# Kernel tuning notes

Hardware: AMD Instinct MI355X
Metric: run time of the kernel (lower is better)

## Reference

```python
import jax, jax.numpy as jnp
import numpy as np

DIM = 2048; H = 16; QLR = 512; KVLR = 512
NOPE = 128; ROPE = 64; VHD = 128
QKHD = NOPE + ROPE
SCALE = QKHD ** -0.5
EPS = 1.1920929e-07  # torch RMSNorm default eps = finfo(float32).eps
B = 1; S = 2048

def _rmsnorm(x, w):
    return x * jax.lax.rsqrt(jnp.mean(x * x, axis=-1, keepdims=True) + EPS) * w

def _rope(x, cos, sin):
    # x: [b, s, h, d]; cos/sin: [s, d//2] (consecutive-pair complex rotation)
    b, s, h, d = x.shape
    x2 = x.reshape(b, s, h, d // 2, 2)
    x0, x1 = x2[..., 0], x2[..., 1]
    c = cos[None, :, None, :]; sn = sin[None, :, None, :]
    y = jnp.stack([x0 * c - x1 * sn, x0 * sn + x1 * c], axis=-1)
    return y.reshape(b, s, h, d)

def setup_inputs() -> dict:
    key = jax.random.key(0)
    ks = jax.random.split(key, 12)
    def lin(k, fan_in, fan_out):
        bound = 1.0 / np.sqrt(fan_in)
        kw, kb = jax.random.split(k)
        w = jax.random.uniform(kw, (fan_out, fan_in), jnp.float32, -bound, bound)
        b = jax.random.uniform(kb, (fan_out,), jnp.float32, -bound, bound)
        return w, b
    x = jax.random.normal(ks[0], (B, S, DIM), jnp.float32)
    theta = jax.random.uniform(ks[1], (S, ROPE // 2), jnp.float32, 0.0, 2 * np.pi)
    freqs_cos = jnp.cos(theta); freqs_sin = jnp.sin(theta)
    mask = jnp.where(jnp.triu(jnp.ones((S, S), bool), k=1), jnp.float32(-1e9), jnp.float32(0.0))
    wq_a_w, wq_a_b = lin(ks[2], DIM, QLR)
    q_norm_w = jnp.ones((QLR,), jnp.float32)
    wq_b_w, wq_b_b = lin(ks[3], QLR, H * QKHD)
    wkv_a_w, wkv_a_b = lin(ks[4], DIM, KVLR + ROPE)
    kv_norm_w = jnp.ones((KVLR,), jnp.float32)
    wkv_b_w, wkv_b_b = lin(ks[5], KVLR, H * (NOPE + VHD))
    wo_w, wo_b = lin(ks[6], H * VHD, DIM)
    return {"x": x, "start_pos": 0, "freqs_cos": freqs_cos, "freqs_sin": freqs_sin,
            "mask": mask, "wq_a_w": wq_a_w, "wq_a_b": wq_a_b, "q_norm_w": q_norm_w,
            "wq_b_w": wq_b_w, "wq_b_b": wq_b_b, "wkv_a_w": wkv_a_w, "wkv_a_b": wkv_a_b,
            "kv_norm_w": kv_norm_w, "wkv_b_w": wkv_b_w, "wkv_b_b": wkv_b_b,
            "wo_w": wo_w, "wo_b": wo_b}

def reference(x, start_pos, freqs_cos, freqs_sin, mask,
              wq_a_w, wq_a_b, q_norm_w, wq_b_w, wq_b_b,
              wkv_a_w, wkv_a_b, kv_norm_w, wkv_b_w, wkv_b_b, wo_w, wo_b):
    bsz, seqlen, _ = x.shape
    # low-rank query: wq_b(q_norm(wq_a(x)))
    q = _rmsnorm(x @ wq_a_w.T + wq_a_b, q_norm_w) @ wq_b_w.T + wq_b_b
    q = q.reshape(bsz, seqlen, H, QKHD)
    q_nope, q_pe = q[..., :NOPE], q[..., NOPE:]
    q_pe = _rope(q_pe, freqs_cos, freqs_sin)
    kv = x @ wkv_a_w.T + wkv_a_b
    kv_lat, k_pe = kv[..., :KVLR], kv[..., KVLR:]
    k_pe = _rope(k_pe[:, :, None, :], freqs_cos, freqs_sin)  # [b,s,1,ROPE]
    q = jnp.concatenate([q_nope, q_pe], axis=-1)
    kvb = (_rmsnorm(kv_lat, kv_norm_w) @ wkv_b_w.T + wkv_b_b).reshape(bsz, seqlen, H, NOPE + VHD)
    k_nope, v = kvb[..., :NOPE], kvb[..., NOPE:]
    k = jnp.concatenate([k_nope, jnp.broadcast_to(k_pe, (bsz, seqlen, H, ROPE))], axis=-1)
    # prefill (start_pos=0): cache[:end_pos] == freshly written k/v
    scores = jnp.einsum('bshd,bthd->bsht', q, k) * SCALE
    scores = scores + mask[None, :, None, :]
    probs = jax.nn.softmax(scores.astype(jnp.float32), axis=-1).astype(x.dtype)
    out = jnp.einsum('bsht,bthd->bshd', probs, v).reshape(bsz, seqlen, H * VHD)
    return out @ wo_w.T + wo_b
```

## Files before the change

### kernel.cpp

```cpp
#include <hip/hip_runtime.h>
#include <hip/hip_bf16.h>

typedef __attribute__((ext_vector_type(8))) short short8x;
typedef __attribute__((ext_vector_type(4))) short short4x;
typedef __attribute__((ext_vector_type(4))) float float4x;
typedef __hip_bfloat16 bf16;

#define EPS_F 1.1920929e-07f
#define SCALE_F 0.07216878364870323f

__device__ inline float rdv(const void* p, size_t i, int f32) {
  return f32 ? ((const float*)p)[i] : __bfloat162float(((const bf16*)p)[i]);
}

__device__ inline int4 pack8(const float* s) {
  unsigned short h[8];
#pragma unroll
  for (int t = 0; t < 8; t++) {
    bf16 b = __float2bfloat16(s[t]);
    __builtin_memcpy(&h[t], &b, 2);
  }
  int4 r;
  r.x = (int)((unsigned)h[0] | ((unsigned)h[1] << 16));
  r.y = (int)((unsigned)h[2] | ((unsigned)h[3] << 16));
  r.z = (int)((unsigned)h[4] | ((unsigned)h[5] << 16));
  r.w = (int)((unsigned)h[6] | ((unsigned)h[7] << 16));
  return r;
}

typedef __attribute__((address_space(1))) const unsigned int gu32;
typedef __attribute__((address_space(3))) unsigned int lu32;
__device__ __forceinline__ void gload16(const void* g, void* l) {
  __builtin_amdgcn_global_load_lds((gu32*)g, (lu32*)l, 16, 0, 0);
}

__global__ __launch_bounds__(256) void detect_dtype(const unsigned short* __restrict__ x,
                                                    int* __restrict__ flag) {
  int tid = threadIdx.x;
  int cnt = 0;
#pragma unroll
  for (int i = 0; i < 4; i++) {
    unsigned short u = x[tid * 4 + i];
    int e = (u >> 7) & 0xFF;
    cnt += (e >= 118 && e <= 130) ? 1 : 0;
  }
#pragma unroll
  for (int off = 1; off < 64; off <<= 1) cnt += __shfl_xor(cnt, off);
  __shared__ int red[4];
  if ((tid & 63) == 0) red[tid >> 6] = cnt;
  __syncthreads();
  if (tid == 0) flag[0] = ((red[0] + red[1] + red[2] + red[3]) > 768) ? 0 : 1;
}

__global__ __launch_bounds__(256) void sentinel_kernel(bf16* out, int n) {
  int i = blockIdx.x * 256 + threadIdx.x;
  if (i < n) out[i] = __float2bfloat16(1000.0f);
}

template<int OMODE, bool A_DYN>
__device__ __forceinline__ void gemm128_body(
    const void* __restrict__ A, const void* __restrict__ W,
    const void* __restrict__ bias, void* __restrict__ Cout,
    int M, int N, int K, int f32in, int bx, int by)
{
  __shared__ int4 As4[128 * 4];
  __shared__ int4 Bs4[128 * 4];
  const int tid = threadIdx.x, lane = tid & 63, wave = tid >> 6;
  const int grp = lane >> 4, l16 = lane & 15;
  const int m0 = bx * 128, n0 = by * 128;
  const int wm = (wave & 1) * 64, wn = (wave >> 1) * 64;
  float4x acc[4][4] = {};
  for (int k0 = 0; k0 < K; k0 += 32) {
    if (!f32in) {
#pragma unroll
      for (int j = 0; j < 2; j++) {
        int row = wave * 32 + j * 16 + (lane >> 2);
        int cs = (lane & 3) ^ ((row >> 1) & 3);
        gload16((const bf16*)A + (size_t)(m0 + row) * K + k0 + cs * 8,
                &As4[(wave * 32 + j * 16) * 4]);
        gload16((const bf16*)W + (size_t)(n0 + row) * K + k0 + cs * 8,
                &Bs4[(wave * 32 + j * 16) * 4]);
      }
    } else {
#pragma unroll
      for (int i = 0; i < 2; i++) {
        int ch = tid + i * 256;
        int row = ch >> 2, c = ch & 3;
        int cs = c ^ ((row >> 1) & 3);
        size_t aoff = (size_t)(m0 + row) * K + k0 + cs * 8;
        size_t boff = (size_t)(n0 + row) * K + k0 + cs * 8;
        As4[row * 4 + c] = A_DYN ? pack8((const float*)A + aoff)
                                 : *(const int4*)((const bf16*)A + aoff);
        Bs4[row * 4 + c] = pack8((const float*)W + boff);
      }
    }
    __syncthreads();
    short8x af[4], bfr[4];
#pragma unroll
    for (int i = 0; i < 4; i++) {
      int ra = wm + i * 16 + l16;
      int rb = wn + i * 16 + l16;
      af[i]  = *(const short8x*)&As4[ra * 4 + (grp ^ ((ra >> 1) & 3))];
      bfr[i] = *(const short8x*)&Bs4[rb * 4 + (grp ^ ((rb >> 1) & 3))];
    }
#pragma unroll
    for (int i = 0; i < 4; i++)
#pragma unroll
      for (int j = 0; j < 4; j++)
        acc[i][j] = __builtin_amdgcn_mfma_f32_16x16x32_bf16(af[i], bfr[j], acc[i][j], 0, 0, 0);
    __syncthreads();
  }
#pragma unroll
  for (int j = 0; j < 4; j++) {
    int gn = n0 + wn + j * 16 + l16;
    float bv = rdv(bias, gn, f32in);
#pragma unroll
    for (int i = 0; i < 4; i++) {
      int gm0 = m0 + wm + i * 16 + grp * 4;
#pragma unroll
      for (int r = 0; r < 4; r++) {
        float v = acc[i][j][r] + bv;
        size_t idx = (size_t)(gm0 + r) * N + gn;
        if (OMODE == 0)      ((float*)Cout)[idx] = v;
        else if (OMODE == 1) ((bf16*)Cout)[idx] = __float2bfloat16(v);
        else {
          if (f32in) ((float*)Cout)[idx] = v;
          else       ((bf16*)Cout)[idx] = __float2bfloat16(v);
        }
      }
    }
  }
}

template<int OMODE, bool A_DYN>
__global__ __launch_bounds__(256) void gemm128(
    const void* __restrict__ A, const void* __restrict__ W,
    const void* __restrict__ bias, void* __restrict__ Cout,
    int M, int N, int K, const int* __restrict__ flagp)
{
  gemm128_body<OMODE, A_DYN>(A, W, bias, Cout, M, N, K, flagp[0],
                             blockIdx.x, blockIdx.y);
}

__global__ __launch_bounds__(256) void gemmB_dual(
    const void* __restrict__ A0, const void* __restrict__ A1,
    const void* __restrict__ W0, const void* __restrict__ W1,
    const void* __restrict__ b0, const void* __restrict__ b1,
    void* __restrict__ C0, void* __restrict__ C1,
    const int* __restrict__ flagp)
{
  const int z = blockIdx.z;
  if (z == 0 && blockIdx.y >= 24) return;
  const void* A = z ? A1 : A0;
  const void* W = z ? W1 : W0;
  const void* bias = z ? b1 : b0;
  void* C = z ? C1 : C0;
  const int N = z ? 4096 : 3072;
  gemm128_body<1, false>(A, W, bias, C, 2048, N, 512, flagp[0],
                         blockIdx.x, blockIdx.y);
}

template<int OMODE, bool A_DYN>
__device__ __forceinline__ void gemm64_body(
    const void* __restrict__ A, const void* __restrict__ W,
    const void* __restrict__ bias, void* __restrict__ Cout,
    int M, int N, int K, int f32in, int bx, int by)
{
  __shared__ int4 As4[64 * 4];
  __shared__ int4 Bs4[64 * 4];
  const int tid = threadIdx.x, lane = tid & 63, wave = tid >> 6;
  const int grp = lane >> 4, l16 = lane & 15;
  const int m0 = bx * 64, n0 = by * 64;
  const int wm = (wave & 1) * 32, wn = (wave >> 1) * 32;
  float4x acc[2][2] = {};
  for (int k0 = 0; k0 < K; k0 += 32) {
    if (!f32in) {
      int row = wave * 16 + (lane >> 2);
      int cs = (lane & 3) ^ ((row >> 1) & 3);
      gload16((const bf16*)A + (size_t)(m0 + row) * K + k0 + cs * 8,
              &As4[wave * 16 * 4]);
      gload16((const bf16*)W + (size_t)(n0 + row) * K + k0 + cs * 8,
              &Bs4[wave * 16 * 4]);
    } else {
      int row = tid >> 2, c = tid & 3;
      int cs = c ^ ((row >> 1) & 3);
      size_t aoff = (size_t)(m0 + row) * K + k0 + cs * 8;
      size_t boff = (size_t)(n0 + row) * K + k0 + cs * 8;
      As4[row * 4 + c] = A_DYN ? pack8((const float*)A + aoff)
                               : *(const int4*)((const bf16*)A + aoff);
      Bs4[row * 4 + c] = pack8((const float*)W + boff);
    }
    __syncthreads();
    short8x af[2], bfr[2];
#pragma unroll
    for (int i = 0; i < 2; i++) {
      int ra = wm + i * 16 + l16;
      int rb = wn + i * 16 + l16;
      af[i]  = *(const short8x*)&As4[ra * 4 + (grp ^ ((ra >> 1) & 3))];
      bfr[i] = *(const short8x*)&Bs4[rb * 4 + (grp ^ ((rb >> 1) & 3))];
    }
#pragma unroll
    for (int i = 0; i < 2; i++)
#pragma unroll
      for (int j = 0; j < 2; j++)
        acc[i][j] = __builtin_amdgcn_mfma_f32_16x16x32_bf16(af[i], bfr[j], acc[i][j], 0, 0, 0);
    __syncthreads();
  }
#pragma unroll
  for (int j = 0; j < 2; j++) {
    int gn = n0 + wn + j * 16 + l16;
    float bv = rdv(bias, gn, f32in);
#pragma unroll
    for (int i = 0; i < 2; i++) {
      int gm0 = m0 + wm + i * 16 + grp * 4;
#pragma unroll
      for (int r = 0; r < 4; r++) {
        float v = acc[i][j][r] + bv;
        size_t idx = (size_t)(gm0 + r) * N + gn;
        if (OMODE == 0)      ((float*)Cout)[idx] = v;
        else if (OMODE == 1) ((bf16*)Cout)[idx] = __float2bfloat16(v);
        else {
          if (f32in) ((float*)Cout)[idx] = v;
          else       ((bf16*)Cout)[idx] = __float2bfloat16(v);
        }
      }
    }
  }
}

__global__ __launch_bounds__(256) void gemmA_dual(
    const void* __restrict__ A,
    const void* __restrict__ W0, const void* __restrict__ W1,
    const void* __restrict__ b0, const void* __restrict__ b1,
    float* __restrict__ C0, float* __restrict__ C1,
    const int* __restrict__ flagp)
{
  const int z = blockIdx.z;
  const int N = z ? 576 : 512;
  if (blockIdx.y * 64 >= N) return;
  const void* W = z ? W1 : W0;
  const void* bias = z ? b1 : b0;
  float* C = z ? C1 : C0;
  gemm64_body<0, true>(A, W, bias, C, 2048, N, 2048, flagp[0],
                       blockIdx.x, blockIdx.y);
}

__global__ __launch_bounds__(256) void norms_merged(
    const float* __restrict__ q_a, const float* __restrict__ kv_a,
    const void* __restrict__ qw, const void* __restrict__ kvw,
    const void* __restrict__ cosb, const void* __restrict__ sinb,
    bf16* __restrict__ qn, bf16* __restrict__ kvn, bf16* __restrict__ kpe,
    const int* __restrict__ flagp)
{
  const int f32in = flagp[0];
  const int b = blockIdx.x, tid = threadIdx.x;
  __shared__ float red[4];
  if (b < 2048) {
    const int s = b;
    const float* row = q_a + (size_t)s * 512;
    float v0 = row[tid], v1 = row[tid + 256];
    float ss = v0 * v0 + v1 * v1;
#pragma unroll
    for (int off = 1; off < 64; off <<= 1) ss += __shfl_xor(ss, off);
    if ((tid & 63) == 0) red[tid >> 6] = ss;
    __syncthreads();
    float tot = red[0] + red[1] + red[2] + red[3];
    float scale = rsqrtf(tot * (1.0f / 512.0f) + EPS_F);
    qn[(size_t)s * 512 + tid]       = __float2bfloat16(v0 * scale * rdv(qw, tid, f32in));
    qn[(size_t)s * 512 + tid + 256] = __float2bfloat16(v1 * scale * rdv(qw, tid + 256, f32in));
  } else {
    const int s = b - 2048;
    const float* row = kv_a + (size_t)s * 576;
    float v0 = row[tid], v1 = row[tid + 256];
    float ss = v0 * v0 + v1 * v1;
#pragma unroll
    for (int off = 1; off < 64; off <<= 1) ss += __shfl_xor(ss, off);
    if ((tid & 63) == 0) red[tid >> 6] = ss;
    __syncthreads();
    float tot = red[0] + red[1] + red[2] + red[3];
    float scale = rsqrtf(tot * (1.0f / 512.0f) + EPS_F);
    kvn[(size_t)s * 512 + tid]       = __float2bfloat16(v0 * scale * rdv(kvw, tid, f32in));
    kvn[(size_t)s * 512 + tid + 256] = __float2bfloat16(v1 * scale * rdv(kvw, tid + 256, f32in));
    if (tid < 32) {
      float x0 = row[512 + 2 * tid], x1 = row[512 + 2 * tid + 1];
      float c  = rdv(cosb, (size_t)s * 32 + tid, f32in);
      float sn = rdv(sinb, (size_t)s * 32 + tid, f32in);
      kpe[s * 64 + 2 * tid]     = __float2bfloat16(x0 * c - x1 * sn);
      kpe[s * 64 + 2 * tid + 1] = __float2bfloat16(x0 * sn + x1 * c);
    }
  }
}

__global__ __launch_bounds__(256) void rope_vt_merged(
    bf16* __restrict__ q, const void* __restrict__ cosb,
    const void* __restrict__ sinb, const bf16* __restrict__ kvb,
    bf16* __restrict__ Vt, const int* __restrict__ flagp)
{
  const int b = blockIdx.x, tid = threadIdx.x;
  __shared__ __align__(16) bf16 tile[64][136];
  if (b < 2048) {
    const int f32in = flagp[0];
    const int s = b;
#pragma unroll
    for (int it = 0; it < 2; it++) {
      int p = tid + it * 256;
      int hh = p >> 5, jj = p & 31;
      bf16* src = q + (size_t)s * 3072 + hh * 192 + 128 + 2 * jj;
      float x0 = __bfloat162float(src[0]);
      float x1 = __bfloat162float(src[1]);
      float c  = rdv(cosb, (size_t)s * 32 + jj, f32in);
      float sn = rdv(sinb, (size_t)s * 32 + jj, f32in);
      src[0] = __float2bfloat16(x0 * c - x1 * sn);
      src[1] = __float2bfloat16(x0 * sn + x1 * c);
    }
  } else {
    const int hb = b - 2048;
    const int h = hb & 15;
    const int t0 = (hb >> 4) * 64;
#pragma unroll
    for (int i = 0; i < 4; i++) {
      int chunk = tid + i * 256;
      int row = chunk >> 4;
      int c8 = (chunk & 15) * 8;
      *(int4*)&tile[row][c8] =
          *(const int4*)(kvb + (size_t)(t0 + row) * 4096 + h * 256 + 128 + c8);
    }
    __syncthreads();
#pragma unroll
    for (int i = 0; i < 32; i++) {
      int idx = tid + i * 256;
      int d = idx >> 6;
      int t = idx & 63;
      Vt[((size_t)h * 128 + d) * 2048 + t0 + t] = tile[t][d];
    }
  }
}

__global__ __launch_bounds__(256) void attn_kernel(
    const bf16* __restrict__ Q, const bf16* __restrict__ kvb,
    const bf16* __restrict__ kpe, const bf16* __restrict__ Vt,
    bf16* __restrict__ Out)
{
  __shared__ __align__(16) bf16 Ks[64 * 200];
  __shared__ __align__(16) bf16 Vs[128 * 72];
  __shared__ __align__(16) bf16 plds[4][16 * 68];
  const int b = blockIdx.x;
  const int h = b & 15;
  const int tt = (b >> 4) & 15;
  const int q0 = ((b >> 8) ? (31 - tt) : tt) * 64;
  const int tid = threadIdx.x;
  const int wave = tid >> 6;
  const int lane = tid & 63;
  const int grp = lane >> 4, l16 = lane & 15;
  const int qrt = q0 + wave * 16;
  const bf16* Qbase = Q + (size_t)(qrt + l16) * 3072 + h * 192;
  short8x qf[6];
#pragma unroll
  for (int c = 0; c < 6; c++)
    qf[c] = *(const short8x*)(Qbase + c * 32 + grp * 8);
  float m_run[4], l_run[4];
  float4x o_acc[8] = {};
#pragma unroll
  for (int r = 0; r < 4; r++) { m_run[r] = -__builtin_inff(); l_run[r] = 0.f; }
  bf16* pl = &plds[wave][0];
  for (int t0 = 0; t0 <= q0; t0 += 64) {
#pragma unroll
    for (int i = 0; i < 4; i++) {
      int ch = tid + i * 256;
      int row = ch >> 4, c = ch & 15;
      *(int4*)&Ks[row * 200 + c * 8] =
          *(const int4*)(kvb + (size_t)(t0 + row) * 4096 + h * 256 + c * 8);
    }
#pragma unroll
    for (int i = 0; i < 2; i++) {
      int ch = tid + i * 256;
      int row = ch >> 3, c = ch & 7;
      *(int4*)&Ks[row * 200 + 128 + c * 8] =
          *(const int4*)(kpe + (size_t)(t0 + row) * 64 + c * 8);
    }
#pragma unroll
    for (int i = 0; i < 4; i++) {
      int ch = tid + i * 256;
      int row = ch >> 3, c = ch & 7;
      *(int4*)&Vs[row * 72 + c * 8] =
          *(const int4*)(Vt + ((size_t)h * 128 + row) * 2048 + t0 + c * 8);
    }
    __syncthreads();
    float4x sacc[4] = {};
#pragma unroll
    for (int n = 0; n < 4; n++) {
      const bf16* Kb = &Ks[(n * 16 + l16) * 200 + grp * 8];
#pragma unroll
      for (int c = 0; c < 6; c++) {
        short8x kf = *(const short8x*)(Kb + c * 32);
        sacc[n] = __builtin_amdgcn_mfma_f32_16x16x32_bf16(qf[c], kf, sacc[n], 0, 0, 0);
      }
    }
    float pv[4][4], alpha[4];
#pragma unroll
    for (int r = 0; r < 4; r++) {
      const int s_row = qrt + grp * 4 + r;
      float p0[4];
      float mx = -__builtin_inff();
#pragma unroll
      for (int n = 0; n < 4; n++) {
        int t = t0 + n * 16 + l16;
        float v = sacc[n][r] * SCALE_F;
        v = (t > s_row) ? -1.0e9f : v;
        p0[n] = v;
        mx = fmaxf(mx, v);
      }
      mx = fmaxf(mx, __shfl_xor(mx, 1));
      mx = fmaxf(mx, __shfl_xor(mx, 2));
      mx = fmaxf(mx, __shfl_xor(mx, 4));
      mx = fmaxf(mx, __shfl_xor(mx, 8));
      float m_new = fmaxf(m_run[r], mx);
      float a = __expf(m_run[r] - m_new);
      m_run[r] = m_new;
      float sum = 0.f;
#pragma unroll
      for (int n = 0; n < 4; n++) {
        float e = __expf(p0[n] - m_new);
        pv[n][r] = e;
        sum += e;
      }
      sum += __shfl_xor(sum, 1);
      sum += __shfl_xor(sum, 2);
      sum += __shfl_xor(sum, 4);
      sum += __shfl_xor(sum, 8);
      l_run[r] = l_run[r] * a + sum;
      alpha[r] = a;
    }
#pragma unroll
    for (int n = 0; n < 8; n++)
#pragma unroll
      for (int r = 0; r < 4; r++)
        o_acc[n][r] *= alpha[r];
#pragma unroll
    for (int n = 0; n < 4; n++)
#pragma unroll
      for (int r = 0; r < 4; r++)
        pl[(grp * 4 + r) * 68 + n * 16 + l16] = __float2bfloat16(pv[n][r]);
#pragma unroll
    for (int c = 0; c < 2; c++) {
      union { short4x h4[2]; short8x v8; } pk;
      const bf16* pp = pl + l16 * 68 + c * 32 + grp * 8;
      pk.h4[0] = *(const short4x*)(pp);
      pk.h4[1] = *(const short4x*)(pp + 4);
#pragma unroll
      for (int n = 0; n < 8; n++) {
        short8x vf = *(const short8x*)&Vs[(size_t)(n * 16 + l16) * 72 + c * 32 + grp * 8];
        o_acc[n] = __builtin_amdgcn_mfma_f32_16x16x32_bf16(pk.v8, vf, o_acc[n], 0, 0, 0);
      }
    }
    __syncthreads();
  }
  float inv[4];
#pragma unroll
  for (int r = 0; r < 4; r++) inv[r] = 1.0f / l_run[r];
#pragma unroll
  for (int n = 0; n < 8; n++)
#pragma unroll
    for (int r = 0; r < 4; r++) {
      int s_row = qrt + grp * 4 + r;
      Out[(size_t)s_row * 2048 + h * 128 + n * 16 + l16] =
          __float2bfloat16(o_acc[n][r] * inv[r]);
    }
}

extern "C" void kernel_launch(void* const* d_in, const int* in_sizes, int n_in,
                              void* d_out, int out_size, void* d_ws, size_t ws_size,
                              hipStream_t stream) {
  const void* x        = d_in[0];
  const void* fcos     = d_in[2];
  const void* fsin     = d_in[3];
  const void* wq_a_w   = d_in[5];
  const void* wq_a_b   = d_in[6];
  const void* q_norm_w = d_in[7];
  const void* wq_b_w   = d_in[8];
  const void* wq_b_b   = d_in[9];
  const void* wkv_a_w  = d_in[10];
  const void* wkv_a_b  = d_in[11];
  const void* kv_norm_w= d_in[12];
  const void* wkv_b_w  = d_in[13];
  const void* wkv_b_b  = d_in[14];
  const void* wo_w     = d_in[15];
  const void* wo_b     = d_in[16];

  const size_t KB = 1024, MB = 1024 * 1024;
  if (ws_size < 46 * MB) {
    sentinel_kernel<<<(out_size + 255) / 256, 256, 0, stream>>>((bf16*)d_out, out_size);
    return;
  }
  char* ws = (char*)d_ws;
  bf16*  kpe    = (bf16*)(ws);
  int*   flag   = (int*)(ws + 256 * KB);
  bf16*  qbuf   = (bf16*)(ws + 512 * KB);
  bf16*  kvb    = (bf16*)(ws + 12 * MB + 512 * KB);
  bf16*  Vt     = (bf16*)(ws + 28 * MB + 512 * KB);
  bf16*  attnout= (bf16*)(ws + 36 * MB + 512 * KB);
  float* q_a    = (float*)(ws + 28 * MB + 512 * KB);
  float* kv_a   = (float*)(ws + 32 * MB + 512 * KB);
  bf16*  qn     = (bf16*)(ws + 37 * MB);
  bf16*  kvn    = (bf16*)(ws + 39 * MB);

  dim3 blk(256);
  detect_dtype<<<1, blk, 0, stream>>>((const unsigned short*)x, flag);
  gemmA_dual<<<dim3(32, 9, 2), blk, 0, stream>>>(
      x, wq_a_w, wkv_a_w, wq_a_b, wkv_a_b, q_a, kv_a, flag);
  norms_merged<<<4096, blk, 0, stream>>>(
      q_a, kv_a, q_norm_w, kv_norm_w, fcos, fsin, qn, kvn, kpe, flag);
  gemmB_dual<<<dim3(16, 32, 2), blk, 0, stream>>>(
      qn, kvn, wq_b_w, wkv_b_w, wq_b_b, wkv_b_b, qbuf, kvb, flag);
  rope_vt_merged<<<2560, blk, 0, stream>>>(qbuf, fcos, fsin, kvb, Vt, flag);
  attn_kernel<<<dim3(512), blk, 0, stream>>>(qbuf, kvb, kpe, Vt, attnout);
  gemm128<2, false><<<dim3(16, 16), blk, 0, stream>>>(
      attnout, wo_w, wo_b, d_out, 2048, 2048, 2048, flag);
}
```

Measured before the change: 384.3 us.

## Split-K the Wo projection and first-stage projections to raise parallelism

Adds k-range and bias-enable parameters to the shared 128- and 64-tile GEMM bodies so one launch can compute two K halves into separate fp32 partial buffers. The output projection now launches twice as many blocks and uses a new reduce kernel that sums the partials, converts the dtype and writes the output. The first x-projection GEMM is split the same way, and the norm kernel sums the two partials as it reads them. The aim is to fill more compute units on the 2048-deep reductions. The cost is extra fp32 partial traffic, one more kernel launch, and a rearranged workspace layout that reuses buffers once they are dead.

```diff
diff --git a/kernel.cpp b/kernel.cpp
--- a/kernel.cpp
+++ b/kernel.cpp
@@ -61,7 +61,8 @@
 __device__ __forceinline__ void gemm128_body(
     const void* __restrict__ A, const void* __restrict__ W,
     const void* __restrict__ bias, void* __restrict__ Cout,
-    int M, int N, int K, int f32in, int bx, int by)
+    int M, int N, int K, int f32in, int bx, int by,
+    int kbeg, int kend, int addbias)
 {
   __shared__ int4 As4[128 * 4];
   __shared__ int4 Bs4[128 * 4];
@@ -70,7 +71,7 @@
   const int m0 = bx * 128, n0 = by * 128;
   const int wm = (wave & 1) * 64, wn = (wave >> 1) * 64;
   float4x acc[4][4] = {};
-  for (int k0 = 0; k0 < K; k0 += 32) {
+  for (int k0 = kbeg; k0 < kend; k0 += 32) {
     if (!f32in) {
 #pragma unroll
       for (int j = 0; j < 2; j++) {
@@ -113,7 +114,7 @@
 #pragma unroll
   for (int j = 0; j < 4; j++) {
     int gn = n0 + wn + j * 16 + l16;
-    float bv = rdv(bias, gn, f32in);
+    float bv = addbias ? rdv(bias, gn, f32in) : 0.0f;
 #pragma unroll
     for (int i = 0; i < 4; i++) {
       int gm0 = m0 + wm + i * 16 + grp * 4;
@@ -132,16 +133,6 @@
   }
 }
 
-template<int OMODE, bool A_DYN>
-__global__ __launch_bounds__(256) void gemm128(
-    const void* __restrict__ A, const void* __restrict__ W,
-    const void* __restrict__ bias, void* __restrict__ Cout,
-    int M, int N, int K, const int* __restrict__ flagp)
-{
-  gemm128_body<OMODE, A_DYN>(A, W, bias, Cout, M, N, K, flagp[0],
-                             blockIdx.x, blockIdx.y);
-}
-
 __global__ __launch_bounds__(256) void gemmB_dual(
     const void* __restrict__ A0, const void* __restrict__ A1,
     const void* __restrict__ W0, const void* __restrict__ W1,
@@ -157,14 +148,50 @@
   void* C = z ? C1 : C0;
   const int N = z ? 4096 : 3072;
   gemm128_body<1, false>(A, W, bias, C, 2048, N, 512, flagp[0],
-                         blockIdx.x, blockIdx.y);
+                         blockIdx.x, blockIdx.y, 0, 512, 1);
+}
+
+__global__ __launch_bounds__(256) void gemmWo_sk(
+    const void* __restrict__ A, const void* __restrict__ W,
+    const void* __restrict__ bias, float* __restrict__ part,
+    const int* __restrict__ flagp)
+{
+  const int z = blockIdx.z;
+  gemm128_body<0, false>(A, W, bias, part + (size_t)z * 2048 * 2048,
+                         2048, 2048, 2048, flagp[0],
+                         blockIdx.x, blockIdx.y, z * 1024, z * 1024 + 1024, z == 0);
+}
+
+__global__ __launch_bounds__(256) void reduce_out(
+    const float* __restrict__ p0, const float* __restrict__ p1,
+    void* __restrict__ out, const int* __restrict__ flagp)
+{
+  const int f32in = flagp[0];
+  size_t i = ((size_t)blockIdx.x * 256 + threadIdx.x) * 4;
+  float4 a = *(const float4*)(p0 + i);
+  float4 b = *(const float4*)(p1 + i);
+  a.x += b.x; a.y += b.y; a.z += b.z; a.w += b.w;
+  if (f32in) {
+    *(float4*)((float*)out + i) = a;
+  } else {
+    unsigned short h[4];
+    bf16 t0 = __float2bfloat16(a.x); __builtin_memcpy(&h[0], &t0, 2);
+    bf16 t1 = __float2bfloat16(a.y); __builtin_memcpy(&h[1], &t1, 2);
+    bf16 t2 = __float2bfloat16(a.z); __builtin_memcpy(&h[2], &t2, 2);
+    bf16 t3 = __float2bfloat16(a.w); __builtin_memcpy(&h[3], &t3, 2);
+    int2 v;
+    v.x = (int)((unsigned)h[0] | ((unsigned)h[1] << 16));
+    v.y = (int)((unsigned)h[2] | ((unsigned)h[3] << 16));
+    *(int2*)((bf16*)out + i) = v;
+  }
 }
 
 template<int OMODE, bool A_DYN>
 __device__ __forceinline__ void gemm64_body(
     const void* __restrict__ A, const void* __restrict__ W,
     const void* __restrict__ bias, void* __restrict__ Cout,
-    int M, int N, int K, int f32in, int bx, int by)
+    int M, int N, int K, int f32in, int bx, int by,
+    int kbeg, int kend, int addbias)
 {
   __shared__ int4 As4[64 * 4];
   __shared__ int4 Bs4[64 * 4];
@@ -173,7 +200,7 @@
   const int m0 = bx * 64, n0 = by * 64;
   const int wm = (wave & 1) * 32, wn = (wave >> 1) * 32;
   float4x acc[2][2] = {};
-  for (int k0 = 0; k0 < K; k0 += 32) {
+  for (int k0 = kbeg; k0 < kend; k0 += 32) {
     if (!f32in) {
       int row = wave * 16 + (lane >> 2);
       int cs = (lane & 3) ^ ((row >> 1) & 3);
@@ -209,7 +236,7 @@
 #pragma unroll
   for (int j = 0; j < 2; j++) {
     int gn = n0 + wn + j * 16 + l16;
-    float bv = rdv(bias, gn, f32in);
+    float bv = addbias ? rdv(bias, gn, f32in) : 0.0f;
 #pragma unroll
     for (int i = 0; i < 2; i++) {
       int gm0 = m0 + wm + i * 16 + grp * 4;
@@ -228,7 +255,7 @@
   }
 }
 
-__global__ __launch_bounds__(256) void gemmA_dual(
+__global__ __launch_bounds__(256) void gemmA_sk(
     const void* __restrict__ A,
     const void* __restrict__ W0, const void* __restrict__ W1,
     const void* __restrict__ b0, const void* __restrict__ b1,
@@ -236,17 +263,20 @@
     const int* __restrict__ flagp)
 {
   const int z = blockIdx.z;
-  const int N = z ? 576 : 512;
+  const int mat = z >> 1, kh = z & 1;
+  const int N = mat ? 576 : 512;
   if (blockIdx.y * 64 >= N) return;
-  const void* W = z ? W1 : W0;
-  const void* bias = z ? b1 : b0;
-  float* C = z ? C1 : C0;
+  const void* W = mat ? W1 : W0;
+  const void* bias = mat ? b1 : b0;
+  float* C = (mat ? C1 : C0) + (size_t)kh * 2048 * N;
   gemm64_body<0, true>(A, W, bias, C, 2048, N, 2048, flagp[0],
-                       blockIdx.x, blockIdx.y);
+                       blockIdx.x, blockIdx.y,
+                       kh * 1024, kh * 1024 + 1024, kh == 0);
 }
 
 __global__ __launch_bounds__(256) void norms_merged(
-    const float* __restrict__ q_a, const float* __restrict__ kv_a,
+    const float* __restrict__ q_a0, const float* __restrict__ q_a1,
+    const float* __restrict__ kv_a0, const float* __restrict__ kv_a1,
     const void* __restrict__ qw, const void* __restrict__ kvw,
     const void* __restrict__ cosb, const void* __restrict__ sinb,
     bf16* __restrict__ qn, bf16* __restrict__ kvn, bf16* __restrict__ kpe,
@@ -257,8 +287,9 @@
   __shared__ float red[4];
   if (b < 2048) {
     const int s = b;
-    const float* row = q_a + (size_t)s * 512;
-    float v0 = row[tid], v1 = row[tid + 256];
+    size_t base = (size_t)s * 512;
+    float v0 = q_a0[base + tid] + q_a1[base + tid];
+    float v1 = q_a0[base + tid + 256] + q_a1[base + tid + 256];
     float ss = v0 * v0 + v1 * v1;
 #pragma unroll
     for (int off = 1; off < 64; off <<= 1) ss += __shfl_xor(ss, off);
@@ -266,12 +297,13 @@
     __syncthreads();
     float tot = red[0] + red[1] + red[2] + red[3];
     float scale = rsqrtf(tot * (1.0f / 512.0f) + EPS_F);
-    qn[(size_t)s * 512 + tid]       = __float2bfloat16(v0 * scale * rdv(qw, tid, f32in));
-    qn[(size_t)s * 512 + tid + 256] = __float2bfloat16(v1 * scale * rdv(qw, tid + 256, f32in));
+    qn[base + tid]       = __float2bfloat16(v0 * scale * rdv(qw, tid, f32in));
+    qn[base + tid + 256] = __float2bfloat16(v1 * scale * rdv(qw, tid + 256, f32in));
   } else {
     const int s = b - 2048;
-    const float* row = kv_a + (size_t)s * 576;
-    float v0 = row[tid], v1 = row[tid + 256];
+    size_t base = (size_t)s * 576;
+    float v0 = kv_a0[base + tid] + kv_a1[base + tid];
+    float v1 = kv_a0[base + tid + 256] + kv_a1[base + tid + 256];
     float ss = v0 * v0 + v1 * v1;
 #pragma unroll
     for (int off = 1; off < 64; off <<= 1) ss += __shfl_xor(ss, off);
@@ -282,7 +314,8 @@
     kvn[(size_t)s * 512 + tid]       = __float2bfloat16(v0 * scale * rdv(kvw, tid, f32in));
     kvn[(size_t)s * 512 + tid + 256] = __float2bfloat16(v1 * scale * rdv(kvw, tid + 256, f32in));
     if (tid < 32) {
-      float x0 = row[512 + 2 * tid], x1 = row[512 + 2 * tid + 1];
+      float x0 = kv_a0[base + 512 + 2 * tid] + kv_a1[base + 512 + 2 * tid];
+      float x1 = kv_a0[base + 512 + 2 * tid + 1] + kv_a1[base + 512 + 2 * tid + 1];
       float c  = rdv(cosb, (size_t)s * 32 + tid, f32in);
       float sn = rdv(sinb, (size_t)s * 32 + tid, f32in);
       kpe[s * 64 + 2 * tid]     = __float2bfloat16(x0 * c - x1 * sn);
@@ -499,21 +532,25 @@
   bf16*  kvb    = (bf16*)(ws + 12 * MB + 512 * KB);
   bf16*  Vt     = (bf16*)(ws + 28 * MB + 512 * KB);
   bf16*  attnout= (bf16*)(ws + 36 * MB + 512 * KB);
-  float* q_a    = (float*)(ws + 28 * MB + 512 * KB);
-  float* kv_a   = (float*)(ws + 32 * MB + 512 * KB);
-  bf16*  qn     = (bf16*)(ws + 37 * MB);
-  bf16*  kvn    = (bf16*)(ws + 39 * MB);
+  float* kv_a0  = (float*)(ws + 512 * KB);
+  float* kv_a1  = (float*)(ws + 5 * MB);
+  float* q_a0   = (float*)(ws + 36 * MB + 512 * KB);
+  float* q_a1   = (float*)(ws + 40 * MB + 512 * KB);
+  bf16*  qn     = (bf16*)(ws + 28 * MB + 512 * KB);
+  bf16*  kvn    = (bf16*)(ws + 30 * MB + 512 * KB);
+  float* wpart  = (float*)(ws + 512 * KB);
 
   dim3 blk(256);
   detect_dtype<<<1, blk, 0, stream>>>((const unsigned short*)x, flag);
-  gemmA_dual<<<dim3(32, 9, 2), blk, 0, stream>>>(
-      x, wq_a_w, wkv_a_w, wq_a_b, wkv_a_b, q_a, kv_a, flag);
+  gemmA_sk<<<dim3(32, 9, 4), blk, 0, stream>>>(
+      x, wq_a_w, wkv_a_w, wq_a_b, wkv_a_b, q_a0, kv_a0, flag);
   norms_merged<<<4096, blk, 0, stream>>>(
-      q_a, kv_a, q_norm_w, kv_norm_w, fcos, fsin, qn, kvn, kpe, flag);
+      q_a0, q_a1, kv_a0, kv_a1, q_norm_w, kv_norm_w, fcos, fsin,
+      qn, kvn, kpe, flag);
   gemmB_dual<<<dim3(16, 32, 2), blk, 0, stream>>>(
       qn, kvn, wq_b_w, wkv_b_w, wq_b_b, wkv_b_b, qbuf, kvb, flag);
   rope_vt_merged<<<2560, blk, 0, stream>>>(qbuf, fcos, fsin, kvb, Vt, flag);
   attn_kernel<<<dim3(512), blk, 0, stream>>>(qbuf, kvb, kpe, Vt, attnout);
-  gemm128<2, false><<<dim3(16, 16), blk, 0, stream>>>(
-      attnout, wo_w, wo_b, d_out, 2048, 2048, 2048, flag);
-}
+  gemmWo_sk<<<dim3(16, 16, 2), blk, 0, stream>>>(attnout, wo_w, wo_b, wpart, flag);
+  reduce_out<<<4096, blk, 0, stream>>>(wpart, wpart + (size_t)2048 * 2048, d_out, flag);
+}
```

After: 345.2 us. 10.2% less time.
